# Optimization experiments

Hardware: AMD Instinct MI355X
Metric: run time of the kernel (lower is better)

## Reference

```python
import jax, jax.numpy as jnp
import numpy as np

EMB_DIM = 1024
N_HEADS = 16
HEAD_DIM = EMB_DIM // N_HEADS


def setup_inputs() -> dict:
    key = jax.random.key(0)
    ks = jax.random.split(key, 6)
    B, S, D = 2, 2048, EMB_DIM
    s = 1.0 / np.sqrt(D)
    return {
        "x": jax.random.normal(ks[0], (B, S, D), dtype=jnp.float32),
        "wq": jax.random.normal(ks[1], (D, D), dtype=jnp.float32) * s,
        "wk": jax.random.normal(ks[2], (D, D), dtype=jnp.float32) * s,
        "wv": jax.random.normal(ks[3], (D, D), dtype=jnp.float32) * s,
        "wo": jax.random.normal(ks[4], (D, D), dtype=jnp.float32) * s,
        "bo": jax.random.normal(ks[5], (D,), dtype=jnp.float32) * 0.01,
    }


def reference(x, wq, wk, wv, wo, bo):
    B, S, D = x.shape
    H, Hd = N_HEADS, HEAD_DIM
    # projections (torch Linear: y = x @ W.T; here weights are stored as [in, out])
    q = (x @ wq).reshape(B, S, H, Hd).transpose(0, 2, 1, 3)  # [B,H,S,Hd]
    k = (x @ wk).reshape(B, S, H, Hd).transpose(0, 2, 1, 3)
    v = (x @ wv).reshape(B, S, H, Hd).transpose(0, 2, 1, 3)
    scores = jnp.einsum("bhqd,bhkd->bhqk", q, k)  # [B,H,S,S]
    causal = jnp.tril(jnp.ones((S, S), dtype=bool))  # keep lower triangle
    scores = jnp.where(causal, scores, -jnp.inf)
    weights = jax.nn.softmax(scores / np.sqrt(Hd), axis=-1)
    ctx = jnp.einsum("bhqk,bhkd->bhqd", weights, v)  # [B,H,S,Hd]
    ctx = ctx.transpose(0, 2, 1, 3).reshape(B, S, D)
    return ctx @ wo + bo
```

## Files before the change

kernel.cpp:

```cpp
#include <hip/hip_runtime.h>
#include <hip/hip_bf16.h>

constexpr int B = 2, S = 2048, D = 1024, H = 16, Hd = 64;
constexpr int M = B * S;
constexpr int K = 1024;

typedef __attribute__((ext_vector_type(8))) short short8;
typedef __attribute__((ext_vector_type(4))) float f32x4;

__device__ __forceinline__ float bf2f(unsigned short u) {
    return __uint_as_float(((unsigned)u) << 16);
}
__device__ __forceinline__ unsigned short f2bf(float f) {
    unsigned u = __float_as_uint(f);
    u += 0x7FFF + ((u >> 16) & 1);
    return (unsigned short)(u >> 16);
}
__device__ __forceinline__ void gload_lds16(const unsigned short* g, unsigned short* l) {
    __builtin_amdgcn_global_load_lds(
        (const __attribute__((address_space(1))) void*)g,
        (__attribute__((address_space(3))) void*)l, 16, 0, 0);
}

__global__ __launch_bounds__(256) void convert_x_kernel(
    const float* __restrict__ x, unsigned short* __restrict__ xb)
{
    const size_t i = ((size_t)blockIdx.x * 256 + threadIdx.x) * 8;
    float4 a = *(const float4*)(x + i), b = *(const float4*)(x + i + 4);
    ushort4 u0 = {f2bf(a.x), f2bf(a.y), f2bf(a.z), f2bf(a.w)};
    ushort4 u1 = {f2bf(b.x), f2bf(b.y), f2bf(b.z), f2bf(b.w)};
    *(ushort4*)(xb + i) = u0;
    *(ushort4*)(xb + i + 4) = u1;
}

__global__ __launch_bounds__(256) void transpose_w_kernel(
    const float* __restrict__ wq, const float* __restrict__ wk,
    const float* __restrict__ wv, const float* __restrict__ wo,
    unsigned short* __restrict__ wqkv_t, unsigned short* __restrict__ wo_t)
{
    __shared__ float tile[64][65];
    const int z = blockIdx.z;
    const float* w = (z == 0) ? wq : (z == 1) ? wk : (z == 2) ? wv : wo;
    unsigned short* dst = (z == 3) ? wo_t : wqkv_t + (size_t)z * K * K;
    const int k0 = blockIdx.x * 64, n0 = blockIdx.y * 64;
    const int t = threadIdx.x;
    #pragma unroll
    for (int it = 0; it < 16; ++it) {
        int idx = t + it * 256;
        tile[idx >> 6][idx & 63] = w[(size_t)(k0 + (idx >> 6)) * K + n0 + (idx & 63)];
    }
    __syncthreads();
    #pragma unroll
    for (int it = 0; it < 16; ++it) {
        int idx = t + it * 256;
        int r = idx >> 6, c = idx & 63;
        dst[(size_t)(n0 + r) * K + k0 + c] = f2bf(tile[c][r]);
    }
}

__global__ __launch_bounds__(256) void qkv_mfma_kernel(
    const unsigned short* __restrict__ xa, const unsigned short* __restrict__ bt,
    unsigned short* __restrict__ q, unsigned short* __restrict__ k,
    unsigned short* __restrict__ vt)
{
    __shared__ unsigned short A_lds[128][32];
    __shared__ unsigned short B_lds[128][32];
    const int t = threadIdx.x, w = t >> 6, l = t & 63;
    const int lr = l & 15, lg = l >> 4;
    const int wm = w >> 1, wn = w & 1;
    const int m0 = blockIdx.x * 128, n0 = blockIdx.y * 128;
    const int srow = l >> 2, skofs = (l & 3) * 8;

    f32x4 acc[4][4];
    #pragma unroll
    for (int i = 0; i < 4; ++i)
        #pragma unroll
        for (int j = 0; j < 4; ++j) acc[i][j] = (f32x4){0.f, 0.f, 0.f, 0.f};

    for (int k0 = 0; k0 < K; k0 += 32) {
        #pragma unroll
        for (int p = 0; p < 2; ++p) {
            const int c = w * 2 + p;
            gload_lds16(xa + (size_t)(m0 + c * 16 + srow) * K + k0 + skofs, &A_lds[c * 16][0]);
            gload_lds16(bt + (size_t)(n0 + c * 16 + srow) * K + k0 + skofs, &B_lds[c * 16][0]);
        }
        __syncthreads();
        short8 af[4], bf[4];
        #pragma unroll
        for (int i = 0; i < 4; ++i) af[i] = *(const short8*)&A_lds[wm * 64 + i * 16 + lr][lg * 8];
        #pragma unroll
        for (int j = 0; j < 4; ++j) bf[j] = *(const short8*)&B_lds[wn * 64 + j * 16 + lr][lg * 8];
        #pragma unroll
        for (int i = 0; i < 4; ++i)
            #pragma unroll
            for (int j = 0; j < 4; ++j)
                acc[i][j] = __builtin_amdgcn_mfma_f32_16x16x32_bf16(af[i], bf[j], acc[i][j], 0, 0, 0);
        __syncthreads();
    }

    const int z = (n0 >> 10);
    const float scale = (z == 0) ? 0.125f : 1.0f;
    #pragma unroll
    for (int i = 0; i < 4; ++i) {
        const int mbase = m0 + wm * 64 + i * 16 + lg * 4;
        #pragma unroll
        for (int j = 0; j < 4; ++j) {
            const int n = n0 + wn * 64 + j * 16 + lr;
            const int nn = n & 1023, hh = nn >> 6, hd = nn & 63;
            #pragma unroll
            for (int r = 0; r < 4; ++r) {
                const int mm = mbase + r, bb = mm >> 11, ss = mm & (S - 1);
                const unsigned short val = f2bf(acc[i][j][r] * scale);
                if (z == 0)      q[((size_t)(bb * H + hh) * S + ss) * Hd + hd] = val;
                else if (z == 1) k[((size_t)(bb * H + hh) * S + ss) * Hd + hd] = val;
                else             vt[((size_t)(bb * H + hh) * Hd + hd) * S + ss] = val;
            }
        }
    }
}

__global__ __launch_bounds__(256) void out_mfma_kernel(
    const unsigned short* __restrict__ a, const unsigned short* __restrict__ bt,
    const float* __restrict__ bias, float* __restrict__ out)
{
    __shared__ unsigned short A_lds[128][32];
    __shared__ unsigned short B_lds[128][32];
    const int t = threadIdx.x, w = t >> 6, l = t & 63;
    const int lr = l & 15, lg = l >> 4;
    const int wm = w >> 1, wn = w & 1;
    const int m0 = blockIdx.x * 128, n0 = blockIdx.y * 128;
    const int srow = l >> 2, skofs = (l & 3) * 8;

    f32x4 acc[4][4];
    #pragma unroll
    for (int i = 0; i < 4; ++i)
        #pragma unroll
        for (int j = 0; j < 4; ++j) acc[i][j] = (f32x4){0.f, 0.f, 0.f, 0.f};

    for (int k0 = 0; k0 < K; k0 += 32) {
        #pragma unroll
        for (int p = 0; p < 2; ++p) {
            const int c = w * 2 + p;
            gload_lds16(a  + (size_t)(m0 + c * 16 + srow) * K + k0 + skofs, &A_lds[c * 16][0]);
            gload_lds16(bt + (size_t)(n0 + c * 16 + srow) * K + k0 + skofs, &B_lds[c * 16][0]);
        }
        __syncthreads();
        short8 af[4], bf[4];
        #pragma unroll
        for (int i = 0; i < 4; ++i) af[i] = *(const short8*)&A_lds[wm * 64 + i * 16 + lr][lg * 8];
        #pragma unroll
        for (int j = 0; j < 4; ++j) bf[j] = *(const short8*)&B_lds[wn * 64 + j * 16 + lr][lg * 8];
        #pragma unroll
        for (int i = 0; i < 4; ++i)
            #pragma unroll
            for (int j = 0; j < 4; ++j)
                acc[i][j] = __builtin_amdgcn_mfma_f32_16x16x32_bf16(af[i], bf[j], acc[i][j], 0, 0, 0);
        __syncthreads();
    }

    #pragma unroll
    for (int i = 0; i < 4; ++i) {
        const int mbase = m0 + wm * 64 + i * 16 + lg * 4;
        #pragma unroll
        for (int j = 0; j < 4; ++j) {
            const int n = n0 + wn * 64 + j * 16 + lr;
            const float bv = bias[n];
            #pragma unroll
            for (int r = 0; r < 4; ++r)
                out[(size_t)(mbase + r) * D + n] = acc[i][j][r] + bv;
        }
    }
}

__device__ __forceinline__ void stage64(const unsigned short* __restrict__ g0,
                                        size_t gstride, unsigned short* lbuf,
                                        int w, int l) {
    #pragma unroll
    for (int it = 0; it < 2; ++it) {
        const int chunk = w * 2 + it;
        const int row = chunk * 8 + (l >> 3);
        const int scol = ((l & 7) ^ (row & 7)) * 8;
        gload_lds16(g0 + (size_t)row * gstride + scol, lbuf + chunk * 512);
    }
}

__global__ __launch_bounds__(256) void attn_mfma_kernel(
    const unsigned short* __restrict__ q, const unsigned short* __restrict__ k,
    const unsigned short* __restrict__ vt, unsigned short* __restrict__ ctx)
{
    __shared__ unsigned short Kb[2][64 * 64];
    __shared__ unsigned short Vb[64 * 64];
    __shared__ unsigned short P_lds[4][16][72];
    const int t = threadIdx.x, w = t >> 6, l = t & 63;
    const int lr = l & 15, lg = l >> 4;
    const int hh = blockIdx.y, bb = blockIdx.z;
    const int qt = (blockIdx.x + 5 * blockIdx.y + 16 * blockIdx.z) & 31;
    const int q0 = qt * 64 + w * 16;
    const int diag = qt;
    const size_t base  = (size_t)(bb * H + hh) * S * Hd;
    const size_t vbase = (size_t)(bb * H + hh) * Hd * S;

    short8 qf[2];
    #pragma unroll
    for (int c = 0; c < 2; ++c)
        qf[c] = *(const short8*)(q + base + (size_t)(q0 + lr) * Hd + c * 32 + lg * 8);

    f32x4 accO[4];
    #pragma unroll
    for (int hb = 0; hb < 4; ++hb) accO[hb] = (f32x4){0.f, 0.f, 0.f, 0.f};
    float m_run = -INFINITY, l_run = 0.f;

    stage64(k + base, Hd, Kb[0], w, l);
    int cur = 0;

    for (int kt = 0; kt <= diag; ++kt) {
        stage64(vt + vbase + (size_t)kt * 64, S, Vb, w, l);
        if (kt < diag) {
            stage64(k + base + (size_t)(kt + 1) * 64 * Hd, Hd, Kb[cur ^ 1], w, l);
            asm volatile("s_waitcnt vmcnt(4)" ::: "memory");
        } else {
            asm volatile("s_waitcnt vmcnt(2)" ::: "memory");
        }
        __builtin_amdgcn_sched_barrier(0);
        __builtin_amdgcn_s_barrier();

        const unsigned short* Kc = Kb[cur];

        f32x4 accS[4];
        #pragma unroll
        for (int kc = 0; kc < 4; ++kc) {
            accS[kc] = (f32x4){0.f, 0.f, 0.f, 0.f};
            const int krow = kc * 16 + lr;
            #pragma unroll
            for (int c = 0; c < 2; ++c) {
                short8 kf = *(const short8*)&Kc[krow * 64 +
                    ((c * 32 + lg * 8) ^ ((krow & 7) * 8))];
                accS[kc] = __builtin_amdgcn_mfma_f32_16x16x32_bf16(kf, qf[c], accS[kc], 0, 0, 0);
            }
        }

        float ps[4][4];
        #pragma unroll
        for (int kc = 0; kc < 4; ++kc)
            #pragma unroll
            for (int r = 0; r < 4; ++r) {
                float s = accS[kc][r];
                if (kt == diag) {
                    if (kc * 16 + lg * 4 + r > w * 16 + lr) s = -INFINITY;
                }
                ps[kc][r] = s;
            }
        float mloc = -INFINITY;
        #pragma unroll
        for (int kc = 0; kc < 4; ++kc)
            #pragma unroll
            for (int r = 0; r < 4; ++r) mloc = fmaxf(mloc, ps[kc][r]);
        mloc = fmaxf(mloc, __shfl_xor(mloc, 16));
        mloc = fmaxf(mloc, __shfl_xor(mloc, 32));
        const float mn = fmaxf(m_run, mloc);
        float rs = 0.f;
        #pragma unroll
        for (int kc = 0; kc < 4; ++kc)
            #pragma unroll
            for (int r = 0; r < 4; ++r) {
                float p = __expf(ps[kc][r] - mn);
                ps[kc][r] = p;
                rs += p;
            }
        rs += __shfl_xor(rs, 16);
        rs += __shfl_xor(rs, 32);
        const float sfc = __expf(m_run - mn);
        l_run = l_run * sfc + rs;
        m_run = mn;
        float sfq[4];
        #pragma unroll
        for (int r = 0; r < 4; ++r) sfq[r] = __shfl(sfc, lg * 4 + r);
        #pragma unroll
        for (int hb = 0; hb < 4; ++hb)
            #pragma unroll
            for (int r = 0; r < 4; ++r) accO[hb][r] *= sfq[r];

        #pragma unroll
        for (int kc = 0; kc < 4; ++kc)
            #pragma unroll
            for (int rp = 0; rp < 2; ++rp)
                *(__hip_bfloat162*)&P_lds[w][lr][kc * 16 + lg * 4 + rp * 2] =
                    __float22bfloat162_rn(make_float2(ps[kc][rp * 2], ps[kc][rp * 2 + 1]));
        short8 pa[2];
        #pragma unroll
        for (int c = 0; c < 2; ++c)
            pa[c] = *(const short8*)&P_lds[w][lr][c * 32 + lg * 8];

        if (kt < diag) asm volatile("s_waitcnt vmcnt(2)" ::: "memory");
        else           asm volatile("s_waitcnt vmcnt(0)" ::: "memory");
        __builtin_amdgcn_sched_barrier(0);
        __builtin_amdgcn_s_barrier();

        #pragma unroll
        for (int hb = 0; hb < 4; ++hb) {
            const int vrow = hb * 16 + lr;
            #pragma unroll
            for (int c = 0; c < 2; ++c) {
                short8 vf = *(const short8*)&Vb[vrow * 64 +
                    ((c * 32 + lg * 8) ^ ((vrow & 7) * 8))];
                accO[hb] = __builtin_amdgcn_mfma_f32_16x16x32_bf16(pa[c], vf, accO[hb], 0, 0, 0);
            }
        }

        __builtin_amdgcn_sched_barrier(0);
        __builtin_amdgcn_s_barrier();
        cur ^= 1;
    }

    const float inv = 1.f / l_run;
    float invq[4];
    #pragma unroll
    for (int r = 0; r < 4; ++r) invq[r] = __shfl(inv, lg * 4 + r);
    #pragma unroll
    for (int r = 0; r < 4; ++r) {
        size_t row = (size_t)(bb * S + q0 + lg * 4 + r) * D + hh * Hd;
        #pragma unroll
        for (int hb = 0; hb < 4; ++hb)
            ctx[row + hb * 16 + lr] = f2bf(accO[hb][r] * invq[r]);
    }
}

extern "C" void kernel_launch(void* const* d_in, const int* in_sizes, int n_in,
                              void* d_out, int out_size, void* d_ws, size_t ws_size,
                              hipStream_t stream) {
    const float* x  = (const float*)d_in[0];
    const float* wq = (const float*)d_in[1];
    const float* wk = (const float*)d_in[2];
    const float* wv = (const float*)d_in[3];
    const float* wo = (const float*)d_in[4];
    const float* bo = (const float*)d_in[5];
    float* out = (float*)d_out;

    char* ws = (char*)d_ws;
    unsigned short* x_bf   = (unsigned short*)ws;
    unsigned short* q      = (unsigned short*)(ws + ((size_t)8  << 20));
    unsigned short* kk     = (unsigned short*)(ws + ((size_t)16 << 20));
    unsigned short* vt     = (unsigned short*)(ws + ((size_t)24 << 20));
    unsigned short* ctx    = x_bf;
    unsigned short* wqkv_t = (unsigned short*)(ws + ((size_t)32 << 20));
    unsigned short* wo_t   = (unsigned short*)(ws + ((size_t)38 << 20));

    convert_x_kernel<<<(M * K) / (256 * 8), 256, 0, stream>>>(x, x_bf);
    dim3 gtr(K / 64, K / 64, 4);
    transpose_w_kernel<<<gtr, 256, 0, stream>>>(wq, wk, wv, wo, wqkv_t, wo_t);

    dim3 gqkv(M / 128, 3072 / 128);
    qkv_mfma_kernel<<<gqkv, 256, 0, stream>>>(x_bf, wqkv_t, q, kk, vt);

    dim3 gattn(S / 64, H, B);
    attn_mfma_kernel<<<gattn, 256, 0, stream>>>(q, kk, vt, ctx);

    dim3 gout(M / 128, D / 128);
    out_mfma_kernel<<<gout, 256, 0, stream>>>(ctx, wo_t, bo, out);
}
```

Before: 129.2 us.

## Load V fragments directly to registers, use exp2 softmax with lazy rescale

The attention kernel now loads V fragments straight from global memory into registers instead of staging them through LDS, which removes one barrier per key tile. Q is pre-scaled by log2(e) in the projection so the softmax can use exp2f. Rescaling is skipped unless the running max grows by more than 8. The patch also adds s_setprio around the MFMA blocks, tree reductions for max and sum, and packed 64-bit P stores. The trade-offs are more VGPR pressure, uncoalesced per-wave V global loads that other waves no longer share, and hand-tuned vmcnt counts that must match the new load counts.

```diff
diff --git a/kernel.cpp b/kernel.cpp
--- a/kernel.cpp
+++ b/kernel.cpp
@@ -99,7 +99,7 @@
     }
 
     const int z = (n0 >> 10);
-    const float scale = (z == 0) ? 0.125f : 1.0f;
+    const float scale = (z == 0) ? 0.125f * 1.44269504f : 1.0f;
     #pragma unroll
     for (int i = 0; i < 4; ++i) {
         const int mbase = m0 + wm * 64 + i * 16 + lg * 4;
@@ -189,7 +189,6 @@
     const unsigned short* __restrict__ vt, unsigned short* __restrict__ ctx)
 {
     __shared__ unsigned short Kb[2][64 * 64];
-    __shared__ unsigned short Vb[64 * 64];
     __shared__ unsigned short P_lds[4][16][72];
     const int t = threadIdx.x, w = t >> 6, l = t & 63;
     const int lr = l & 15, lg = l >> 4;
@@ -214,19 +213,28 @@
     int cur = 0;
 
     for (int kt = 0; kt <= diag; ++kt) {
-        stage64(vt + vbase + (size_t)kt * 64, S, Vb, w, l);
+        short8 vf[4][2];
+        #pragma unroll
+        for (int hb = 0; hb < 4; ++hb)
+            #pragma unroll
+            for (int c = 0; c < 2; ++c)
+                vf[hb][c] = *(const short8*)(vt + vbase +
+                    (size_t)(hb * 16 + lr) * S + kt * 64 + c * 32 + lg * 8);
+
         if (kt < diag) {
             stage64(k + base + (size_t)(kt + 1) * 64 * Hd, Hd, Kb[cur ^ 1], w, l);
-            asm volatile("s_waitcnt vmcnt(4)" ::: "memory");
+            asm volatile("s_waitcnt vmcnt(10)" ::: "memory");
         } else {
-            asm volatile("s_waitcnt vmcnt(2)" ::: "memory");
+            asm volatile("s_waitcnt vmcnt(8)" ::: "memory");
         }
         __builtin_amdgcn_sched_barrier(0);
         __builtin_amdgcn_s_barrier();
+        asm volatile("" ::: "memory");
 
         const unsigned short* Kc = Kb[cur];
 
         f32x4 accS[4];
+        __builtin_amdgcn_s_setprio(1);
         #pragma unroll
         for (int kc = 0; kc < 4; ++kc) {
             accS[kc] = (f32x4){0.f, 0.f, 0.f, 0.f};
@@ -238,54 +246,63 @@
                 accS[kc] = __builtin_amdgcn_mfma_f32_16x16x32_bf16(kf, qf[c], accS[kc], 0, 0, 0);
             }
         }
-
-        float ps[4][4];
+        __builtin_amdgcn_s_setprio(0);
+
+        float ps[16];
         #pragma unroll
         for (int kc = 0; kc < 4; ++kc)
             #pragma unroll
             for (int r = 0; r < 4; ++r) {
                 float s = accS[kc][r];
-                if (kt == diag) {
-                    if (kc * 16 + lg * 4 + r > w * 16 + lr) s = -INFINITY;
-                }
-                ps[kc][r] = s;
+                if (kt == diag && (kc * 16 + lg * 4 + r > w * 16 + lr)) s = -INFINITY;
+                ps[kc * 4 + r] = s;
             }
-        float mloc = -INFINITY;
-        #pragma unroll
-        for (int kc = 0; kc < 4; ++kc)
-            #pragma unroll
-            for (int r = 0; r < 4; ++r) mloc = fmaxf(mloc, ps[kc][r]);
+        float m8[8];
+        #pragma unroll
+        for (int i = 0; i < 8; ++i) m8[i] = fmaxf(ps[i], ps[i + 8]);
+        float m4a = fmaxf(m8[0], m8[4]), m4b = fmaxf(m8[1], m8[5]);
+        float m4c = fmaxf(m8[2], m8[6]), m4d = fmaxf(m8[3], m8[7]);
+        float mloc = fmaxf(fmaxf(m4a, m4b), fmaxf(m4c, m4d));
         mloc = fmaxf(mloc, __shfl_xor(mloc, 16));
         mloc = fmaxf(mloc, __shfl_xor(mloc, 32));
-        const float mn = fmaxf(m_run, mloc);
-        float rs = 0.f;
-        #pragma unroll
-        for (int kc = 0; kc < 4; ++kc)
-            #pragma unroll
-            for (int r = 0; r < 4; ++r) {
-                float p = __expf(ps[kc][r] - mn);
-                ps[kc][r] = p;
-                rs += p;
-            }
+
+        const bool resc = __any(mloc > m_run + 8.f);
+        const float mn = resc ? fmaxf(m_run, mloc) : m_run;
+
+        #pragma unroll
+        for (int i = 0; i < 16; ++i) ps[i] = exp2f(ps[i] - mn);
+        float s8[8];
+        #pragma unroll
+        for (int i = 0; i < 8; ++i) s8[i] = ps[i] + ps[i + 8];
+        float rs = ((s8[0] + s8[4]) + (s8[1] + s8[5])) +
+                   ((s8[2] + s8[6]) + (s8[3] + s8[7]));
         rs += __shfl_xor(rs, 16);
         rs += __shfl_xor(rs, 32);
-        const float sfc = __expf(m_run - mn);
-        l_run = l_run * sfc + rs;
-        m_run = mn;
-        float sfq[4];
-        #pragma unroll
-        for (int r = 0; r < 4; ++r) sfq[r] = __shfl(sfc, lg * 4 + r);
-        #pragma unroll
-        for (int hb = 0; hb < 4; ++hb)
-            #pragma unroll
-            for (int r = 0; r < 4; ++r) accO[hb][r] *= sfq[r];
-
-        #pragma unroll
-        for (int kc = 0; kc < 4; ++kc)
-            #pragma unroll
-            for (int rp = 0; rp < 2; ++rp)
-                *(__hip_bfloat162*)&P_lds[w][lr][kc * 16 + lg * 4 + rp * 2] =
-                    __float22bfloat162_rn(make_float2(ps[kc][rp * 2], ps[kc][rp * 2 + 1]));
+
+        if (resc) {
+            const float sfc = exp2f(m_run - mn);
+            l_run = l_run * sfc + rs;
+            m_run = mn;
+            float sfq[4];
+            #pragma unroll
+            for (int r = 0; r < 4; ++r) sfq[r] = __shfl(sfc, lg * 4 + r);
+            #pragma unroll
+            for (int hb = 0; hb < 4; ++hb)
+                #pragma unroll
+                for (int r = 0; r < 4; ++r) accO[hb][r] *= sfq[r];
+        } else {
+            l_run += rs;
+        }
+
+        #pragma unroll
+        for (int kc = 0; kc < 4; ++kc) {
+            uint2 pk;
+            *(__hip_bfloat162*)&pk.x =
+                __float22bfloat162_rn(make_float2(ps[kc * 4 + 0], ps[kc * 4 + 1]));
+            *(__hip_bfloat162*)&pk.y =
+                __float22bfloat162_rn(make_float2(ps[kc * 4 + 2], ps[kc * 4 + 3]));
+            *(uint2*)&P_lds[w][lr][kc * 16 + lg * 4] = pk;
+        }
         short8 pa[2];
         #pragma unroll
         for (int c = 0; c < 2; ++c)
@@ -293,22 +310,18 @@
 
         if (kt < diag) asm volatile("s_waitcnt vmcnt(2)" ::: "memory");
         else           asm volatile("s_waitcnt vmcnt(0)" ::: "memory");
+        __builtin_amdgcn_s_setprio(1);
+        #pragma unroll
+        for (int hb = 0; hb < 4; ++hb)
+            #pragma unroll
+            for (int c = 0; c < 2; ++c)
+                accO[hb] = __builtin_amdgcn_mfma_f32_16x16x32_bf16(pa[c], vf[hb][c], accO[hb], 0, 0, 0);
+        __builtin_amdgcn_s_setprio(0);
+
+        asm volatile("" ::: "memory");
         __builtin_amdgcn_sched_barrier(0);
         __builtin_amdgcn_s_barrier();
-
-        #pragma unroll
-        for (int hb = 0; hb < 4; ++hb) {
-            const int vrow = hb * 16 + lr;
-            #pragma unroll
-            for (int c = 0; c < 2; ++c) {
-                short8 vf = *(const short8*)&Vb[vrow * 64 +
-                    ((c * 32 + lg * 8) ^ ((vrow & 7) * 8))];
-                accO[hb] = __builtin_amdgcn_mfma_f32_16x16x32_bf16(pa[c], vf, accO[hb], 0, 0, 0);
-            }
-        }
-
-        __builtin_amdgcn_sched_barrier(0);
-        __builtin_amdgcn_s_barrier();
+        asm volatile("" ::: "memory");
         cur ^= 1;
     }
 
```

Measured after the change: 168.8 us. 1.31x slower.
